# Kernel optimization log

Measured on AMD Instinct MI355X. Metric: run time of the kernel, lower is better.

## Reference

```python
import jax, jax.numpy as jnp
import numpy as np


def _gcn_norm(edge_index, num_nodes):
    # PyG GCNConv default: add self-loops, symmetric normalization.
    src, dst = edge_index[0], edge_index[1]
    loop = jnp.arange(num_nodes, dtype=edge_index.dtype)
    src = jnp.concatenate([src, loop])
    dst = jnp.concatenate([dst, loop])
    deg = jax.ops.segment_sum(jnp.ones_like(dst, dtype=jnp.float32), dst,
                              num_segments=num_nodes)
    dinv = jnp.where(deg > 0, jax.lax.rsqrt(deg), 0.0)
    norm = dinv[src] * dinv[dst]  # [E + N]
    return src, dst, norm


def _gcn_conv(x, src, dst, norm, W, b):
    h = x @ W                      # [N, F_out]
    msg = h[src] * norm[:, None]   # gather + scale, [E+N, F_out]
    agg = jax.ops.segment_sum(msg, dst, num_segments=x.shape[0])
    return agg + b


def reference(x, edge_index, W1, b1, W2, b2, Wfc, bfc):
    N = x.shape[0]
    src, dst, norm = _gcn_norm(edge_index, N)
    h = jax.nn.relu(_gcn_conv(x, src, dst, norm, W1, b1))
    h = jax.nn.relu(_gcn_conv(h, src, dst, norm, W2, b2))
    return h @ Wfc + bfc  # [N, 2]


def setup_inputs() -> dict:
    N, E, D, OUT = 50000, 800000, 128, 2
    key = jax.random.key(0)
    ks = jax.random.split(key, 6)
    s = 1.0 / np.sqrt(D)
    return {
        "x": jax.random.normal(ks[0], (N, D), dtype=jnp.float32),
        "edge_index": jax.random.randint(ks[1], (2, E), 0, N, dtype=jnp.int32),
        "W1": jax.random.normal(ks[2], (D, D), dtype=jnp.float32) * s,
        "b1": jnp.zeros((D,), dtype=jnp.float32),
        "W2": jax.random.normal(ks[3], (D, D), dtype=jnp.float32) * s,
        "b2": jnp.zeros((D,), dtype=jnp.float32),
        "Wfc": jax.random.normal(ks[4], (D, OUT), dtype=jnp.float32) * s,
        "bfc": jnp.zeros((OUT,), dtype=jnp.float32),
    }
```

## Files before the change

### kernel.cpp

```cpp
#include <hip/hip_runtime.h>
#include <hip/hip_fp16.h>

#define D 128
#define GEMM_TM 64
#define EDGE_BLOCKS 2048
#define CAP 64

typedef _Float16 f16x8 __attribute__((ext_vector_type(8)));
typedef float f32x4 __attribute__((ext_vector_type(4)));

__device__ __forceinline__ void stage_wt(const float* __restrict__ W, f16x8* wt) {
#pragma unroll
    for (int i = 0; i < 8; ++i) {
        int u = i * 256 + threadIdx.x;
        int c = u & 127;
        int k0 = (u >> 7) * 8;
        f16x8 v;
#pragma unroll
        for (int j = 0; j < 8; ++j) v[j] = (_Float16)W[(k0 + j) * D + c];
        wt[u] = v;
    }
}

__device__ __forceinline__ void mfma_rows(const f16x8 af[4], const f16x8* wt,
                                          __half* __restrict__ Y,
                                          int row_base, int N, int lane) {
    int kg = lane >> 4;
    int c15 = lane & 15;
#pragma unroll
    for (int ct = 0; ct < 8; ++ct) {
        f32x4 acc = {0.f, 0.f, 0.f, 0.f};
#pragma unroll
        for (int ks = 0; ks < 4; ++ks) {
            f16x8 bf = wt[(ks * 4 + kg) * 128 + ct * 16 + c15];
            acc = __builtin_amdgcn_mfma_f32_16x16x32_f16(af[ks], bf, acc, 0, 0, 0);
        }
        int c = ct * 16 + c15;
#pragma unroll
        for (int r = 0; r < 4; ++r) {
            int grow = row_base + kg * 4 + r;
            if (grow < N) Y[(size_t)grow * D + c] = __float2half(acc[r]);
        }
    }
}

__global__ __launch_bounds__(256) void k_gemm1_bin(const float* __restrict__ X,
                                                   const float* __restrict__ W1,
                                                   __half* __restrict__ T1,
                                                   int gblocks, int NV,
                                                   const int* __restrict__ src,
                                                   const int* __restrict__ dst,
                                                   int* __restrict__ fill,
                                                   unsigned short* __restrict__ col,
                                                   int E) {
    __shared__ f16x8 wt[2048];
    int b = blockIdx.x;
    if (b >= gblocks) {
        int w = b - gblocks;
        int r = b & 7;
        int lo = (r * NV) >> 3;
        int hi = ((r + 1) * NV) >> 3;
        int idx = (w >> 3) * 256 + threadIdx.x;
        int stride = (EDGE_BLOCKS / 8) * 256;
        for (int e = idx; e < E; e += stride) {
            int d = dst[e];
            if (d >= lo && d < hi) {
                int s = src[e];
                int pos = atomicAdd(&fill[d], 1);
                if (pos < CAP) col[(size_t)d * CAP + pos] = (unsigned short)s;
            }
        }
        return;
    }
    stage_wt(W1, wt);
    __syncthreads();

    int lane = threadIdx.x & 63, w = threadIdx.x >> 6;
    int tile_row = b * GEMM_TM + w * 16;
    int ar = tile_row + (lane & 15);
    const float* xr = X + (size_t)(ar < NV ? ar : NV - 1) * D;
    int kg = lane >> 4;
    f16x8 af[4];
#pragma unroll
    for (int ks = 0; ks < 4; ++ks) {
        float4 lo4 = *(const float4*)(xr + ks * 32 + kg * 8);
        float4 hi4 = *(const float4*)(xr + ks * 32 + kg * 8 + 4);
        f16x8 v = {(_Float16)lo4.x, (_Float16)lo4.y, (_Float16)lo4.z, (_Float16)lo4.w,
                   (_Float16)hi4.x, (_Float16)hi4.y, (_Float16)hi4.z, (_Float16)hi4.w};
        af[ks] = v;
    }
    mfma_rows(af, wt, T1, tile_row, NV, lane);
}

__global__ __launch_bounds__(256) void k_gemm2(const __half* __restrict__ H,
                                               const float* __restrict__ W2,
                                               __half* __restrict__ T2, int N) {
    __shared__ f16x8 wt[2048];
    stage_wt(W2, wt);
    __syncthreads();

    int lane = threadIdx.x & 63, w = threadIdx.x >> 6;
    int tile_row = blockIdx.x * GEMM_TM + w * 16;
    int ar = tile_row + (lane & 15);
    const __half* hr = H + (size_t)(ar < N ? ar : N - 1) * D;
    int kg = lane >> 4;
    f16x8 af[4];
#pragma unroll
    for (int ks = 0; ks < 4; ++ks)
        af[ks] = *(const f16x8*)(hr + ks * 32 + kg * 8);
    mfma_rows(af, wt, T2, tile_row, N, lane);
}

__device__ __forceinline__ float2 agg_gather(const __half* __restrict__ T,
                                             const int* __restrict__ fill,
                                             const unsigned short* __restrict__ col,
                                             int n, int lane, float* dn_out) {
    const __half2* __restrict__ Tv = (const __half2*)T;
    int deg = fill[n];
    float dn = rsqrtf((float)(deg + 1));
    *dn_out = dn;
    float2 self = __half22float2(Tv[(size_t)n * 64 + lane]);
    float ax = dn * self.x, ay = dn * self.y;
    int e = n * CAP;
    int end = e + (deg < CAP ? deg : CAP);
    for (; e + 8 <= end; e += 8) {
        int s0 = __builtin_amdgcn_readfirstlane((int)col[e]);
        int s1 = __builtin_amdgcn_readfirstlane((int)col[e + 1]);
        int s2 = __builtin_amdgcn_readfirstlane((int)col[e + 2]);
        int s3 = __builtin_amdgcn_readfirstlane((int)col[e + 3]);
        int s4 = __builtin_amdgcn_readfirstlane((int)col[e + 4]);
        int s5 = __builtin_amdgcn_readfirstlane((int)col[e + 5]);
        int s6 = __builtin_amdgcn_readfirstlane((int)col[e + 6]);
        int s7 = __builtin_amdgcn_readfirstlane((int)col[e + 7]);
        float d0 = rsqrtf((float)(fill[s0] + 1));
        float d1 = rsqrtf((float)(fill[s1] + 1));
        float d2 = rsqrtf((float)(fill[s2] + 1));
        float d3 = rsqrtf((float)(fill[s3] + 1));
        float d4 = rsqrtf((float)(fill[s4] + 1));
        float d5 = rsqrtf((float)(fill[s5] + 1));
        float d6 = rsqrtf((float)(fill[s6] + 1));
        float d7 = rsqrtf((float)(fill[s7] + 1));
        float2 v0 = __half22float2(Tv[(size_t)s0 * 64 + lane]);
        float2 v1 = __half22float2(Tv[(size_t)s1 * 64 + lane]);
        float2 v2 = __half22float2(Tv[(size_t)s2 * 64 + lane]);
        float2 v3 = __half22float2(Tv[(size_t)s3 * 64 + lane]);
        float2 v4 = __half22float2(Tv[(size_t)s4 * 64 + lane]);
        float2 v5 = __half22float2(Tv[(size_t)s5 * 64 + lane]);
        float2 v6 = __half22float2(Tv[(size_t)s6 * 64 + lane]);
        float2 v7 = __half22float2(Tv[(size_t)s7 * 64 + lane]);
        ax = fmaf(d0, v0.x, ax); ay = fmaf(d0, v0.y, ay);
        ax = fmaf(d1, v1.x, ax); ay = fmaf(d1, v1.y, ay);
        ax = fmaf(d2, v2.x, ax); ay = fmaf(d2, v2.y, ay);
        ax = fmaf(d3, v3.x, ax); ay = fmaf(d3, v3.y, ay);
        ax = fmaf(d4, v4.x, ax); ay = fmaf(d4, v4.y, ay);
        ax = fmaf(d5, v5.x, ax); ay = fmaf(d5, v5.y, ay);
        ax = fmaf(d6, v6.x, ax); ay = fmaf(d6, v6.y, ay);
        ax = fmaf(d7, v7.x, ax); ay = fmaf(d7, v7.y, ay);
    }
    for (; e < end; ++e) {
        int s = __builtin_amdgcn_readfirstlane((int)col[e]);
        float ds = rsqrtf((float)(fill[s] + 1));
        float2 v = __half22float2(Tv[(size_t)s * 64 + lane]);
        ax = fmaf(ds, v.x, ax); ay = fmaf(ds, v.y, ay);
    }
    return {ax, ay};
}

__global__ __launch_bounds__(256) void agg_relu(const __half* __restrict__ T,
                                                const int* __restrict__ fill,
                                                const unsigned short* __restrict__ col,
                                                const float* __restrict__ bias,
                                                __half* __restrict__ H, int N) {
    int n = (blockIdx.x * blockDim.x + threadIdx.x) >> 6;
    int lane = threadIdx.x & 63;
    if (n >= N) return;
    n = __builtin_amdgcn_readfirstlane(n);
    float dn;
    float2 a = agg_gather(T, fill, col, n, lane, &dn);
    float2 b = ((const float2*)bias)[lane];
    float hx = fmaxf(fmaf(dn, a.x, b.x), 0.f);
    float hy = fmaxf(fmaf(dn, a.y, b.y), 0.f);
    ((__half2*)H)[(size_t)n * 64 + lane] = __floats2half2_rn(hx, hy);
}

__global__ __launch_bounds__(256) void agg_fc(const __half* __restrict__ T,
                                              const int* __restrict__ fill,
                                              const unsigned short* __restrict__ col,
                                              const float* __restrict__ b2,
                                              const float* __restrict__ Wfc,
                                              const float* __restrict__ bfc,
                                              float* __restrict__ out, int N) {
    int n = (blockIdx.x * blockDim.x + threadIdx.x) >> 6;
    int lane = threadIdx.x & 63;
    if (n >= N) return;
    n = __builtin_amdgcn_readfirstlane(n);
    float dn;
    float2 a = agg_gather(T, fill, col, n, lane, &dn);
    float2 b = ((const float2*)b2)[lane];
    float hx = fmaxf(fmaf(dn, a.x, b.x), 0.f);
    float hy = fmaxf(fmaf(dn, a.y, b.y), 0.f);
    float2 w0 = ((const float2*)Wfc)[2 * lane];
    float2 w1 = ((const float2*)Wfc)[2 * lane + 1];
    float o0 = hx * w0.x + hy * w1.x;
    float o1 = hx * w0.y + hy * w1.y;
#pragma unroll
    for (int off = 32; off > 0; off >>= 1) {
        o0 += __shfl_down(o0, off);
        o1 += __shfl_down(o1, off);
    }
    if (lane == 0) {
        out[(size_t)n * 2 + 0] = o0 + bfc[0];
        out[(size_t)n * 2 + 1] = o1 + bfc[1];
    }
}


extern "C" void kernel_launch(void* const* d_in, const int* in_sizes, int n_in,
                              void* d_out, int out_size, void* d_ws, size_t ws_size,
                              hipStream_t stream) {
    const float* x   = (const float*)d_in[0];
    const int* ei    = (const int*)d_in[1];
    const float* W1  = (const float*)d_in[2];
    const float* b1  = (const float*)d_in[3];
    const float* W2  = (const float*)d_in[4];
    const float* b2  = (const float*)d_in[5];
    const float* Wfc = (const float*)d_in[6];
    const float* bfc = (const float*)d_in[7];
    float* out = (float*)d_out;

    const int N = in_sizes[0] / D;
    const int E = in_sizes[1] / 2;
    const int* src = ei;
    const int* dst = ei + E;

    __half* t1  = (__half*)d_ws;
    __half* h16 = t1 + (size_t)N * D;
    __half* t2  = h16 + (size_t)N * D;
    int* fill   = (int*)(t2 + (size_t)N * D);
    unsigned short* col = (unsigned short*)(fill + N);

    hipMemsetAsync(fill, 0, (size_t)N * sizeof(int), stream);

    int gblocks = (int)((N + GEMM_TM - 1) / GEMM_TM);

    k_gemm1_bin<<<gblocks + EDGE_BLOCKS, 256, 0, stream>>>(
        x, W1, t1, gblocks, N, src, dst, fill, col, E);

    int ablocks = (N + 3) / 4;
    agg_relu<<<ablocks, 256, 0, stream>>>(t1, fill, col, b1, h16, N);

    k_gemm2<<<gblocks, 256, 0, stream>>>(h16, W2, t2, N);

    agg_fc<<<ablocks, 256, 0, stream>>>(t2, fill, col, b2, Wfc, bfc, out, N);
}
```

Before: 157.6 us.

## Split wavefront into four edge groups with 16-byte feature loads in aggregation

The aggregation kernels stop walking edges serially with the whole wavefront reading one half2 per lane. Each wave is now split into four 16-lane groups, and every group handles a different neighbor per step with 16-byte f16x8 loads, covering 8 edges per iteration. Partial sums are combined with cross-lane shuffles, and the final FC reduction uses xor shuffles within 16 lanes. This is meant to put more independent gathers in flight and use wider loads, at the cost of predicated tail handling and a cross-group reduction.

```diff
diff --git a/kernel.cpp b/kernel.cpp
--- a/kernel.cpp
+++ b/kernel.cpp
@@ -111,59 +111,42 @@
     mfma_rows(af, wt, T2, tile_row, N, lane);
 }
 
-__device__ __forceinline__ float2 agg_gather(const __half* __restrict__ T,
-                                             const int* __restrict__ fill,
-                                             const unsigned short* __restrict__ col,
-                                             int n, int lane, float* dn_out) {
-    const __half2* __restrict__ Tv = (const __half2*)T;
-    int deg = fill[n];
-    float dn = rsqrtf((float)(deg + 1));
-    *dn_out = dn;
-    float2 self = __half22float2(Tv[(size_t)n * 64 + lane]);
-    float ax = dn * self.x, ay = dn * self.y;
-    int e = n * CAP;
-    int end = e + (deg < CAP ? deg : CAP);
-    for (; e + 8 <= end; e += 8) {
-        int s0 = __builtin_amdgcn_readfirstlane((int)col[e]);
-        int s1 = __builtin_amdgcn_readfirstlane((int)col[e + 1]);
-        int s2 = __builtin_amdgcn_readfirstlane((int)col[e + 2]);
-        int s3 = __builtin_amdgcn_readfirstlane((int)col[e + 3]);
-        int s4 = __builtin_amdgcn_readfirstlane((int)col[e + 4]);
-        int s5 = __builtin_amdgcn_readfirstlane((int)col[e + 5]);
-        int s6 = __builtin_amdgcn_readfirstlane((int)col[e + 6]);
-        int s7 = __builtin_amdgcn_readfirstlane((int)col[e + 7]);
-        float d0 = rsqrtf((float)(fill[s0] + 1));
-        float d1 = rsqrtf((float)(fill[s1] + 1));
-        float d2 = rsqrtf((float)(fill[s2] + 1));
-        float d3 = rsqrtf((float)(fill[s3] + 1));
-        float d4 = rsqrtf((float)(fill[s4] + 1));
-        float d5 = rsqrtf((float)(fill[s5] + 1));
-        float d6 = rsqrtf((float)(fill[s6] + 1));
-        float d7 = rsqrtf((float)(fill[s7] + 1));
-        float2 v0 = __half22float2(Tv[(size_t)s0 * 64 + lane]);
-        float2 v1 = __half22float2(Tv[(size_t)s1 * 64 + lane]);
-        float2 v2 = __half22float2(Tv[(size_t)s2 * 64 + lane]);
-        float2 v3 = __half22float2(Tv[(size_t)s3 * 64 + lane]);
-        float2 v4 = __half22float2(Tv[(size_t)s4 * 64 + lane]);
-        float2 v5 = __half22float2(Tv[(size_t)s5 * 64 + lane]);
-        float2 v6 = __half22float2(Tv[(size_t)s6 * 64 + lane]);
-        float2 v7 = __half22float2(Tv[(size_t)s7 * 64 + lane]);
-        ax = fmaf(d0, v0.x, ax); ay = fmaf(d0, v0.y, ay);
-        ax = fmaf(d1, v1.x, ax); ay = fmaf(d1, v1.y, ay);
-        ax = fmaf(d2, v2.x, ax); ay = fmaf(d2, v2.y, ay);
-        ax = fmaf(d3, v3.x, ax); ay = fmaf(d3, v3.y, ay);
-        ax = fmaf(d4, v4.x, ax); ay = fmaf(d4, v4.y, ay);
-        ax = fmaf(d5, v5.x, ax); ay = fmaf(d5, v5.y, ay);
-        ax = fmaf(d6, v6.x, ax); ay = fmaf(d6, v6.y, ay);
-        ax = fmaf(d7, v7.x, ax); ay = fmaf(d7, v7.y, ay);
-    }
-    for (; e < end; ++e) {
-        int s = __builtin_amdgcn_readfirstlane((int)col[e]);
-        float ds = rsqrtf((float)(fill[s] + 1));
-        float2 v = __half22float2(Tv[(size_t)s * 64 + lane]);
-        ax = fmaf(ds, v.x, ax); ay = fmaf(ds, v.y, ay);
-    }
-    return {ax, ay};
+__device__ __forceinline__ void agg_core(const __half* __restrict__ T,
+                                         const int* __restrict__ fill,
+                                         const unsigned short* __restrict__ col,
+                                         int n, int lane, int deg,
+                                         float acc[8]) {
+    int l4 = lane & 15;
+    int g = lane >> 4;
+#pragma unroll
+    for (int j = 0; j < 8; ++j) acc[j] = 0.f;
+    int base = n * CAP;
+    int dcap = deg < CAP ? deg : CAP;
+    int last = base + dcap - 1;
+
+    for (int it = 0; it < dcap; it += 8) {
+        int ei0 = it + g;
+        int ei1 = it + 4 + g;
+        bool a0 = ei0 < dcap, a1 = ei1 < dcap;
+        int e0 = a0 ? base + ei0 : last;
+        int e1 = a1 ? base + ei1 : last;
+        int s0 = (int)col[e0];
+        int s1 = (int)col[e1];
+        float w0 = a0 ? rsqrtf((float)(fill[s0] + 1)) : 0.f;
+        float w1 = a1 ? rsqrtf((float)(fill[s1] + 1)) : 0.f;
+        f16x8 v0 = *(const f16x8*)(T + (size_t)s0 * D + l4 * 8);
+        f16x8 v1 = *(const f16x8*)(T + (size_t)s1 * D + l4 * 8);
+#pragma unroll
+        for (int j = 0; j < 8; ++j) {
+            acc[j] = fmaf(w0, (float)v0[j], acc[j]);
+            acc[j] = fmaf(w1, (float)v1[j], acc[j]);
+        }
+    }
+#pragma unroll
+    for (int j = 0; j < 8; ++j) {
+        acc[j] += __shfl_down(acc[j], 32);
+        acc[j] += __shfl_down(acc[j], 16);
+    }
 }
 
 __global__ __launch_bounds__(256) void agg_relu(const __half* __restrict__ T,
@@ -175,12 +158,24 @@
     int lane = threadIdx.x & 63;
     if (n >= N) return;
     n = __builtin_amdgcn_readfirstlane(n);
-    float dn;
-    float2 a = agg_gather(T, fill, col, n, lane, &dn);
-    float2 b = ((const float2*)bias)[lane];
-    float hx = fmaxf(fmaf(dn, a.x, b.x), 0.f);
-    float hy = fmaxf(fmaf(dn, a.y, b.y), 0.f);
-    ((__half2*)H)[(size_t)n * 64 + lane] = __floats2half2_rn(hx, hy);
+    int deg = fill[n];
+    float dn = rsqrtf((float)(deg + 1));
+    float acc[8];
+    agg_core(T, fill, col, n, lane, deg, acc);
+    if (lane < 16) {
+        int l4 = lane;
+        f16x8 self = *(const f16x8*)(T + (size_t)n * D + l4 * 8);
+        f32x4 b0 = *(const f32x4*)(bias + l4 * 8);
+        f32x4 b1 = *(const f32x4*)(bias + l4 * 8 + 4);
+        f16x8 o;
+#pragma unroll
+        for (int j = 0; j < 8; ++j) {
+            float t = acc[j] + dn * (float)self[j];
+            float bj = (j < 4) ? b0[j] : b1[j - 4];
+            o[j] = (_Float16)fmaxf(fmaf(dn, t, bj), 0.f);
+        }
+        *(f16x8*)(H + (size_t)n * D + l4 * 8) = o;
+    }
 }
 
 __global__ __launch_bounds__(256) void agg_fc(const __half* __restrict__ T,
@@ -194,19 +189,28 @@
     int lane = threadIdx.x & 63;
     if (n >= N) return;
     n = __builtin_amdgcn_readfirstlane(n);
-    float dn;
-    float2 a = agg_gather(T, fill, col, n, lane, &dn);
-    float2 b = ((const float2*)b2)[lane];
-    float hx = fmaxf(fmaf(dn, a.x, b.x), 0.f);
-    float hy = fmaxf(fmaf(dn, a.y, b.y), 0.f);
-    float2 w0 = ((const float2*)Wfc)[2 * lane];
-    float2 w1 = ((const float2*)Wfc)[2 * lane + 1];
-    float o0 = hx * w0.x + hy * w1.x;
-    float o1 = hx * w0.y + hy * w1.y;
-#pragma unroll
-    for (int off = 32; off > 0; off >>= 1) {
-        o0 += __shfl_down(o0, off);
-        o1 += __shfl_down(o1, off);
+    int deg = fill[n];
+    float dn = rsqrtf((float)(deg + 1));
+    float acc[8];
+    agg_core(T, fill, col, n, lane, deg, acc);
+    int l4 = lane & 15;
+    f16x8 self = *(const f16x8*)(T + (size_t)n * D + l4 * 8);
+    f32x4 b0 = *(const f32x4*)(b2 + l4 * 8);
+    f32x4 b1 = *(const f32x4*)(b2 + l4 * 8 + 4);
+    float o0 = 0.f, o1 = 0.f;
+#pragma unroll
+    for (int j = 0; j < 8; ++j) {
+        float t = acc[j] + dn * (float)self[j];
+        float bj = (j < 4) ? b0[j] : b1[j - 4];
+        float h = fmaxf(fmaf(dn, t, bj), 0.f);
+        float2 wf = ((const float2*)Wfc)[l4 * 8 + j];
+        o0 = fmaf(h, wf.x, o0);
+        o1 = fmaf(h, wf.y, o1);
+    }
+#pragma unroll
+    for (int off = 8; off > 0; off >>= 1) {
+        o0 += __shfl_xor(o0, off);
+        o1 += __shfl_xor(o1, off);
     }
     if (lane == 0) {
         out[(size_t)n * 2 + 0] = o0 + bfc[0];
```

Measured after the change: 142.5 us. 9.5% less time.
